# Performance work log

Measured on AMD Instinct MI355X. Metric: run time of the kernel, lower is better.

The kernel has to match this reference:

```python
import jax, jax.numpy as jnp
import numpy as np

TEMPERATURE = 0.5  # init kwarg: temperature
EPS = 1e-8         # torch CosineSimilarity eps


def setup_inputs() -> dict:
    key = jax.random.key(0)
    k1, k2 = jax.random.split(key)
    B, D = 2048, 256
    return {
        "z_i": jax.random.normal(k1, (B, D), dtype=jnp.float32),
        "z_j": jax.random.normal(k2, (B, D), dtype=jnp.float32),
    }


def reference(z_i, z_j):
    # NT-Xent (SimCLR) loss, world_size = 1.
    B = z_i.shape[0]
    N = 2 * B
    z = jnp.concatenate([z_i, z_j], axis=0)                       # [N, D]
    # Cosine similarity = normalized dot product (fused normalize + matmul,
    # avoiding the torch broadcast NxNxD intermediate).
    zn = z / jnp.clip(jnp.linalg.norm(z, axis=1, keepdims=True), EPS)
    sim = (zn @ zn.T) / TEMPERATURE                               # [N, N]
    # Positive pair similarity for each row: diag offsets +B and -B.
    pos = jnp.concatenate([jnp.diagonal(sim, offset=B),
                           jnp.diagonal(sim, offset=-B)], axis=0)  # [N]
    # CrossEntropy with label 0 over logits [pos, negatives] equals
    # -pos + logsumexp over {pos} U negatives = all off-diagonal entries,
    # since the mask removes exactly the diagonal and the positive pair
    # (which is re-added as `pos`). Mask diagonal with -inf.
    neg_inf = jnp.finfo(sim.dtype).min
    sim_masked = jnp.where(jnp.eye(N, dtype=bool), neg_inf, sim)
    lse = jax.scipy.special.logsumexp(sim_masked, axis=1)          # [N]
    # reduction='sum' then / N  ->  mean over rows
    loss = jnp.sum(lse - pos) / N
    return loss
```

## Files before the change

kernel.cpp:

```cpp
#include <hip/hip_runtime.h>


#define NROWS 4096
#define DDIM 256
#define BHALF 2048
#define TILE 128
#define BK 64
#define LDP 72
#define NCB (NROWS / TILE)
#define INV_T 2.0f

typedef short bf16x8 __attribute__((ext_vector_type(8)));
typedef float f32x4 __attribute__((ext_vector_type(4)));

__device__ inline unsigned short f2bf(float f) {
    union { float f; unsigned u; } c; c.f = f;
    unsigned u = c.u + 0x7fffu + ((c.u >> 16) & 1u);
    return (unsigned short)(u >> 16);
}

__global__ __launch_bounds__(256) void k_normalize(
    const float* __restrict__ zi, const float* __restrict__ zj,
    unsigned short* __restrict__ zn) {
    const int wave = threadIdx.x >> 6, lane = threadIdx.x & 63;
    const int row = blockIdx.x * 4 + wave;
    const float* src = (row < BHALF) ? (zi + row * DDIM)
                                     : (zj + (row - BHALF) * DDIM);
    const float4 v = ((const float4*)src)[lane];
    float ss = v.x * v.x + v.y * v.y + v.z * v.z + v.w * v.w;
    #pragma unroll
    for (int m = 1; m < 64; m <<= 1) ss += __shfl_xor(ss, m);
    const float scale = 1.0f / fmaxf(sqrtf(ss), 1e-8f);
    ushort4 o;
    o.x = f2bf(v.x * scale); o.y = f2bf(v.y * scale);
    o.z = f2bf(v.z * scale); o.w = f2bf(v.w * scale);
    ((ushort4*)(zn + row * DDIM))[lane] = o;
}

__global__ __launch_bounds__(256) void k_simlse(
    const unsigned short* __restrict__ zn,
    float* __restrict__ partial,
    float* __restrict__ posv) {
    __shared__ unsigned short As[TILE * LDP];
    __shared__ unsigned short Bs[TILE * LDP];
    __shared__ float pscratch[TILE];

    const int tid = threadIdx.x;
    const int wave = tid >> 6, lane = tid & 63;
    const int quad = lane >> 4, l15 = lane & 15;
    const int wr = wave >> 1, wc = wave & 1;
    const int rowBase = blockIdx.x * TILE;
    const int colBase = blockIdx.y * TILE;

    f32x4 acc[4][4] = {};

    for (int kb = 0; kb < DDIM / BK; ++kb) {
        __syncthreads();
        #pragma unroll
        for (int i = 0; i < 4; ++i) {
            const int flat = tid + i * 256;
            const int r = flat >> 3, c = flat & 7;
            *(bf16x8*)&As[r * LDP + c * 8] =
                *(const bf16x8*)&zn[(rowBase + r) * DDIM + kb * BK + c * 8];
            *(bf16x8*)&Bs[r * LDP + c * 8] =
                *(const bf16x8*)&zn[(colBase + r) * DDIM + kb * BK + c * 8];
        }
        __syncthreads();
        #pragma unroll
        for (int s = 0; s < 2; ++s) {
            bf16x8 af[4], bf[4];
            #pragma unroll
            for (int mt = 0; mt < 4; ++mt)
                af[mt] = *(const bf16x8*)&As[(wr * 64 + mt * 16 + l15) * LDP + s * 32 + quad * 8];
            #pragma unroll
            for (int nt = 0; nt < 4; ++nt)
                bf[nt] = *(const bf16x8*)&Bs[(wc * 64 + nt * 16 + l15) * LDP + s * 32 + quad * 8];
            #pragma unroll
            for (int mt = 0; mt < 4; ++mt)
                #pragma unroll
                for (int nt = 0; nt < 4; ++nt)
                    acc[mt][nt] = __builtin_amdgcn_mfma_f32_16x16x32_bf16(
                        af[mt], bf[nt], acc[mt][nt], 0, 0, 0);
        }
    }

    float ssum[4][4];
    #pragma unroll
    for (int mt = 0; mt < 4; ++mt) {
        #pragma unroll
        for (int r = 0; r < 4; ++r) {
            const int grow = rowBase + wr * 64 + mt * 16 + quad * 4 + r;
            float s = 0.f;
            #pragma unroll
            for (int nt = 0; nt < 4; ++nt) {
                const int gcol = colBase + wc * 64 + nt * 16 + l15;
                const float simv = acc[mt][nt][r] * INV_T;
                if (gcol != grow) s += __expf(simv);
                if (gcol == grow + BHALF || grow == gcol + BHALF)
                    posv[grow] = simv;
            }
            s += __shfl_xor(s, 1); s += __shfl_xor(s, 2);
            s += __shfl_xor(s, 4); s += __shfl_xor(s, 8);
            ssum[mt][r] = s;
        }
    }
    __syncthreads();
    if (wc == 0 && l15 == 0) {
        #pragma unroll
        for (int mt = 0; mt < 4; ++mt)
            #pragma unroll
            for (int r = 0; r < 4; ++r)
                pscratch[wr * 64 + mt * 16 + quad * 4 + r] = ssum[mt][r];
    }
    __syncthreads();
    if (wc == 1 && l15 == 0) {
        #pragma unroll
        for (int mt = 0; mt < 4; ++mt)
            #pragma unroll
            for (int r = 0; r < 4; ++r) {
                const int lr = wr * 64 + mt * 16 + quad * 4 + r;
                partial[blockIdx.y * NROWS + rowBase + lr] =
                    ssum[mt][r] + pscratch[lr];
            }
    }
}

__global__ __launch_bounds__(256) void k_rowlse(
    const float* __restrict__ partial, const float* __restrict__ posv,
    float* __restrict__ blocksum) {
    __shared__ float red[4];
    const int tid = threadIdx.x;
    const int row = blockIdx.x * 256 + tid;
    float s = 0.f;
    #pragma unroll
    for (int p = 0; p < NCB; ++p) s += partial[p * NROWS + row];
    float v = __logf(s) - posv[row];
    #pragma unroll
    for (int m = 1; m < 64; m <<= 1) v += __shfl_xor(v, m);
    if ((tid & 63) == 0) red[tid >> 6] = v;
    __syncthreads();
    if (tid == 0)
        blocksum[blockIdx.x] = red[0] + red[1] + red[2] + red[3];
}

__global__ __launch_bounds__(64) void k_final2(
    const float* __restrict__ blocksum, float* __restrict__ out) {
    const int lane = threadIdx.x;
    float v = (lane < 16) ? blocksum[lane] : 0.f;
    #pragma unroll
    for (int m = 1; m < 16; m <<= 1) v += __shfl_xor(v, m);
    if (lane == 0) out[0] = v * (1.0f / (float)NROWS);
}

extern "C" void kernel_launch(void* const* d_in, const int* in_sizes, int n_in,
                              void* d_out, int out_size, void* d_ws, size_t ws_size,
                              hipStream_t stream) {
    const float* zi = (const float*)d_in[0];
    const float* zj = (const float*)d_in[1];
    float* out = (float*)d_out;

    unsigned short* zn = (unsigned short*)d_ws;
    float* partial = (float*)((char*)d_ws + NROWS * DDIM * 2);
    float* posv = partial + NCB * NROWS;
    float* blocksum = posv + NROWS;

    k_normalize<<<NROWS / 4, 256, 0, stream>>>(zi, zj, zn);
    k_simlse<<<dim3(NROWS / TILE, NROWS / TILE), 256, 0, stream>>>(zn, partial, posv);
    k_rowlse<<<16, 256, 0, stream>>>(partial, posv, blocksum);
    k_final2<<<1, 64, 0, stream>>>(blocksum, out);
}
```

Baseline: 82.11 us.

## Exploit symmetry of similarity matrix by computing only upper-triangular tiles

The similarity kernel now launches only the upper-triangular tile pairs and decodes (bx, by) from a linear block index. Each tile contributes row sums and also column sums, which are written as the partial sums of the transposed tile, so the matmul and exp work is roughly halved. The cost is extra column reductions and shuffles per tile, a small decode loop at block start, and a less even load across blocks.

```diff
diff --git a/kernel.cpp b/kernel.cpp
--- a/kernel.cpp
+++ b/kernel.cpp
@@ -44,16 +44,22 @@
     __shared__ unsigned short As[TILE * LDP];
     __shared__ unsigned short Bs[TILE * LDP];
     __shared__ float pscratch[TILE];
+    __shared__ float cscratch[TILE];
+
+    int t = blockIdx.x, bx = 0, rem = NCB;
+    while (t >= rem) { t -= rem; ++bx; --rem; }
+    const int by = bx + t;
 
     const int tid = threadIdx.x;
     const int wave = tid >> 6, lane = tid & 63;
     const int quad = lane >> 4, l15 = lane & 15;
     const int wr = wave >> 1, wc = wave & 1;
-    const int rowBase = blockIdx.x * TILE;
-    const int colBase = blockIdx.y * TILE;
+    const int rowBase = bx * TILE;
+    const int colBase = by * TILE;
 
     f32x4 acc[4][4] = {};
 
+    #pragma unroll
     for (int kb = 0; kb < DDIM / BK; ++kb) {
         __syncthreads();
         #pragma unroll
@@ -84,7 +90,8 @@
         }
     }
 
-    float ssum[4][4];
+    float rsum[4][4];
+    float csum[4] = {};
     #pragma unroll
     for (int mt = 0; mt < 4; ++mt) {
         #pragma unroll
@@ -95,22 +102,37 @@
             for (int nt = 0; nt < 4; ++nt) {
                 const int gcol = colBase + wc * 64 + nt * 16 + l15;
                 const float simv = acc[mt][nt][r] * INV_T;
-                if (gcol != grow) s += __expf(simv);
-                if (gcol == grow + BHALF || grow == gcol + BHALF)
+                const float e = (gcol != grow) ? __expf(simv) : 0.f;
+                s += e;
+                csum[nt] += e;
+                if (gcol == grow + BHALF) {
                     posv[grow] = simv;
+                    posv[gcol] = simv;
+                }
             }
             s += __shfl_xor(s, 1); s += __shfl_xor(s, 2);
             s += __shfl_xor(s, 4); s += __shfl_xor(s, 8);
-            ssum[mt][r] = s;
+            rsum[mt][r] = s;
         }
     }
+    #pragma unroll
+    for (int nt = 0; nt < 4; ++nt) {
+        csum[nt] += __shfl_xor(csum[nt], 16);
+        csum[nt] += __shfl_xor(csum[nt], 32);
+    }
+
     __syncthreads();
     if (wc == 0 && l15 == 0) {
         #pragma unroll
         for (int mt = 0; mt < 4; ++mt)
             #pragma unroll
             for (int r = 0; r < 4; ++r)
-                pscratch[wr * 64 + mt * 16 + quad * 4 + r] = ssum[mt][r];
+                pscratch[wr * 64 + mt * 16 + quad * 4 + r] = rsum[mt][r];
+    }
+    if (wr == 0 && quad == 0) {
+        #pragma unroll
+        for (int nt = 0; nt < 4; ++nt)
+            cscratch[wc * 64 + nt * 16 + l15] = csum[nt];
     }
     __syncthreads();
     if (wc == 1 && l15 == 0) {
@@ -119,9 +141,15 @@
             #pragma unroll
             for (int r = 0; r < 4; ++r) {
                 const int lr = wr * 64 + mt * 16 + quad * 4 + r;
-                partial[blockIdx.y * NROWS + rowBase + lr] =
-                    ssum[mt][r] + pscratch[lr];
+                partial[by * NROWS + rowBase + lr] = rsum[mt][r] + pscratch[lr];
             }
+    }
+    if (bx != by && wr == 1 && quad == 0) {
+        #pragma unroll
+        for (int nt = 0; nt < 4; ++nt) {
+            const int lc = wc * 64 + nt * 16 + l15;
+            partial[bx * NROWS + colBase + lc] = csum[nt] + cscratch[lc];
+        }
     }
 }
 
@@ -165,7 +193,7 @@
     float* blocksum = posv + NROWS;
 
     k_normalize<<<NROWS / 4, 256, 0, stream>>>(zi, zj, zn);
-    k_simlse<<<dim3(NROWS / TILE, NROWS / TILE), 256, 0, stream>>>(zn, partial, posv);
+    k_simlse<<<NCB * (NCB + 1) / 2, 256, 0, stream>>>(zn, partial, posv);
     k_rowlse<<<16, 256, 0, stream>>>(partial, posv, blocksum);
     k_final2<<<1, 64, 0, stream>>>(blocksum, out);
 }
```

After: 80.09 us. 2.5% less time.
